# Kernel tuning notes

Hardware: AMD Instinct MI355X
Metric: run time of the kernel (lower is better)

Reference implementation:

```python
import jax, jax.numpy as jnp
import numpy as np

B, S = 4096, 4096
TAU = 0.95
METRIC = 'f1'


def setup_inputs() -> dict:
    key = jax.random.key(0)
    k1, k2 = jax.random.split(key)
    # predicted per-position probabilities, kept strictly positive for log()
    output = jax.random.uniform(k1, (B, S, 1), dtype=jnp.float32, minval=1e-3, maxval=1.0)
    labels = (jax.random.uniform(k2, (B, S)) < 0.2).astype(jnp.float32)
    return {"output": output, "labels": labels}


def _metric_weights(labels):
    # cutoff j keeps documents [0..j] -> prefix statistics via a single cumsum per row
    tp = jnp.cumsum(labels, axis=1)                      # true positives at each cutoff, [B,S]
    if METRIC == 'f1':
        k = jnp.arange(1, labels.shape[1] + 1, dtype=labels.dtype)  # cutoff sizes 1..S
        prec = tp / k                                    # [B,S]
        total = jnp.sum(labels, axis=1, keepdims=True)   # [B,1]
        rec = jnp.where(total > 0, tp / jnp.maximum(total, 1.0), 0.0)
        denom = prec + rec
        r = jnp.where(denom > 0, 2.0 * prec * rec / jnp.maximum(denom, 1e-30), 0.0)
    else:  # dcg
        pos = jnp.arange(labels.shape[1], dtype=labels.dtype)
        gains = labels / jnp.log2(pos + 2.0)             # gain of doc at rank i
        r = jnp.cumsum(gains, axis=1)                    # dcg@(j+1), [B,S]
    return r


def reference(output, labels):
    r = _metric_weights(labels)                          # [B,S]
    q = jnp.exp(r / TAU)                                 # [B,S]
    norm_factor = jnp.sum(q, axis=1, keepdims=True)      # [B,1]
    # NOTE: faithful to original code: q is overwritten with 1/norm_factor
    w = 1.0 / norm_factor                                # [B,1]
    log_out = jnp.log(jnp.squeeze(output, axis=2))       # [B,S]
    loss_matrix = log_out * w                            # broadcast [B,S]*[B,1]
    return -jnp.sum(loss_matrix) / output.shape[0]
```

## Files before the change

### kernel.cpp

```cpp
#include <hip/hip_runtime.h>


#define BDIM 256
#define VPT 16
#define SROW 4096
#define NROWS 4096

__global__ __launch_bounds__(BDIM) void attncut_row_kernel(
    const float* __restrict__ output,
    const float* __restrict__ labels,
    float* __restrict__ row_out)
{
    const int b    = blockIdx.x;
    const int tid  = threadIdx.x;
    const int lane = tid & 63;
    const int wave = tid >> 6;
    const int base = tid * VPT;

    const float* lab = labels + (size_t)b * SROW + base;
    const float* out = output + (size_t)b * SROW + base;

    float4 Lv[4], Ov[4];
    #pragma unroll
    for (int i = 0; i < 4; ++i) Lv[i] = reinterpret_cast<const float4*>(lab)[i];
    #pragma unroll
    for (int i = 0; i < 4; ++i) Ov[i] = reinterpret_cast<const float4*>(out)[i];

    float v[VPT], o[VPT];
    #pragma unroll
    for (int i = 0; i < 4; ++i) {
        v[4*i+0] = Lv[i].x; v[4*i+1] = Lv[i].y; v[4*i+2] = Lv[i].z; v[4*i+3] = Lv[i].w;
        o[4*i+0] = Ov[i].x; o[4*i+1] = Ov[i].y; o[4*i+2] = Ov[i].z; o[4*i+3] = Ov[i].w;
    }

    float pre[VPT];
    float acc = 0.f;
    #pragma unroll
    for (int i = 0; i < VPT; ++i) { acc += v[i]; pre[i] = acc; }
    const float cnt = acc;

    float lsum = 0.f;
    #pragma unroll
    for (int i = 0; i < VPT; ++i) lsum += __logf(o[i]);

    float sc = cnt;
    #pragma unroll
    for (int d = 1; d < 64; d <<= 1) {
        float n = __shfl_up(sc, d, 64);
        if (lane >= d) sc += n;
    }

    __shared__ float wtot[4], wpre[4];
    __shared__ float s_total;
    if (lane == 63) wtot[wave] = sc;
    __syncthreads();
    if (tid == 0) {
        float a = 0.f;
        #pragma unroll
        for (int w = 0; w < 4; ++w) { wpre[w] = a; a += wtot[w]; }
        s_total = a;
    }
    __syncthreads();
    const float total = s_total;
    const float excl  = wpre[wave] + (sc - cnt);

    const float c = 2.0f / 0.95f;
    float qsum = 0.f;
    #pragma unroll
    for (int i = 0; i < VPT; ++i) {
        float tp = excl + pre[i];
        float kf = (float)(base + i + 1) + total;
        qsum += __expf(c * tp * __builtin_amdgcn_rcpf(kf));
    }

    #pragma unroll
    for (int d = 32; d > 0; d >>= 1) {
        qsum += __shfl_down(qsum, d, 64);
        lsum += __shfl_down(lsum, d, 64);
    }
    __shared__ float sq[4], sl[4];
    if (lane == 0) { sq[wave] = qsum; sl[wave] = lsum; }
    __syncthreads();
    if (tid == 0) {
        float Q = 0.f, L = 0.f;
        #pragma unroll
        for (int w = 0; w < 4; ++w) { Q += sq[w]; L += sl[w]; }
        row_out[b] = L / Q;
    }
}

__global__ __launch_bounds__(1024) void attncut_final_kernel(
    const float* __restrict__ row_out, float* __restrict__ d_out)
{
    const int tid = threadIdx.x;
    float s = 0.f;
    for (int i = tid; i < NROWS; i += 1024) s += row_out[i];
    #pragma unroll
    for (int d = 32; d > 0; d >>= 1) s += __shfl_down(s, d, 64);
    __shared__ float sm[16];
    const int lane = tid & 63, wave = tid >> 6;
    if (lane == 0) sm[wave] = s;
    __syncthreads();
    if (tid == 0) {
        float t = 0.f;
        #pragma unroll
        for (int w = 0; w < 16; ++w) t += sm[w];
        d_out[0] = -t / (float)NROWS;
    }
}

extern "C" void kernel_launch(void* const* d_in, const int* in_sizes, int n_in,
                              void* d_out, int out_size, void* d_ws, size_t ws_size,
                              hipStream_t stream) {
    const float* output = (const float*)d_in[0];
    const float* labels = (const float*)d_in[1];
    float* out  = (float*)d_out;
    float* rows = (float*)d_ws;

    attncut_row_kernel<<<NROWS, BDIM, 0, stream>>>(output, labels, rows);
    attncut_final_kernel<<<1, 1024, 0, stream>>>(rows, out);
}
```

Measured before the change: 28.26 us.

## Use one wave per row with ballot/mbcnt prefix counts instead of block scan

Each row is now handled by a single 64-lane wavefront that reads 16 coalesced float4 chunks, strided so the wave covers contiguous 1 KB spans. The labels' prefix sums are computed with ballot and mbcnt bit counts, which removes the shuffle scan, shared memory and both block barriers. The output loads are split into two halves so the second half is fetched while the exp work runs. The trade-off is more registers per thread and fewer threads per row, and the ballot-based count assumes the labels are exactly 0 or 1.

```diff
diff --git a/kernel.cpp b/kernel.cpp
--- a/kernel.cpp
+++ b/kernel.cpp
@@ -1,92 +1,92 @@
 #include <hip/hip_runtime.h>
 
 
-#define BDIM 256
-#define VPT 16
 #define SROW 4096
 #define NROWS 4096
+#define NCHUNK 16
 
-__global__ __launch_bounds__(BDIM) void attncut_row_kernel(
+__global__ __launch_bounds__(64, 4) void attncut_row_kernel(
     const float* __restrict__ output,
     const float* __restrict__ labels,
     float* __restrict__ row_out)
 {
     const int b    = blockIdx.x;
-    const int tid  = threadIdx.x;
-    const int lane = tid & 63;
-    const int wave = tid >> 6;
-    const int base = tid * VPT;
+    const int lane = threadIdx.x;
 
-    const float* lab = labels + (size_t)b * SROW + base;
-    const float* out = output + (size_t)b * SROW + base;
+    const float4* lab4 = reinterpret_cast<const float4*>(labels) + (size_t)b * (SROW / 4) + lane;
+    const float4* out4 = reinterpret_cast<const float4*>(output) + (size_t)b * (SROW / 4) + lane;
 
-    float4 Lv[4], Ov[4];
+    float4 L[NCHUNK];
     #pragma unroll
-    for (int i = 0; i < 4; ++i) Lv[i] = reinterpret_cast<const float4*>(lab)[i];
+    for (int c = 0; c < NCHUNK; ++c) L[c] = lab4[c * 64];
+
+    float4 O0[8];
     #pragma unroll
-    for (int i = 0; i < 4; ++i) Ov[i] = reinterpret_cast<const float4*>(out)[i];
+    for (int c = 0; c < 8; ++c) O0[c] = out4[c * 64];
 
-    float v[VPT], o[VPT];
+    float T[NCHUNK][4];
+    float P[NCHUNK];
+    unsigned int run = 0;
     #pragma unroll
-    for (int i = 0; i < 4; ++i) {
-        v[4*i+0] = Lv[i].x; v[4*i+1] = Lv[i].y; v[4*i+2] = Lv[i].z; v[4*i+3] = Lv[i].w;
-        o[4*i+0] = Ov[i].x; o[4*i+1] = Ov[i].y; o[4*i+2] = Ov[i].z; o[4*i+3] = Ov[i].w;
+    for (int c = 0; c < NCHUNK; ++c) {
+        unsigned long long b0 = __ballot(L[c].x > 0.5f);
+        unsigned long long b1 = __ballot(L[c].y > 0.5f);
+        unsigned long long b2 = __ballot(L[c].z > 0.5f);
+        unsigned long long b3 = __ballot(L[c].w > 0.5f);
+        unsigned int acc = __builtin_amdgcn_mbcnt_lo((unsigned int)b0, 0u);
+        acc = __builtin_amdgcn_mbcnt_hi((unsigned int)(b0 >> 32), acc);
+        acc = __builtin_amdgcn_mbcnt_lo((unsigned int)b1, acc);
+        acc = __builtin_amdgcn_mbcnt_hi((unsigned int)(b1 >> 32), acc);
+        acc = __builtin_amdgcn_mbcnt_lo((unsigned int)b2, acc);
+        acc = __builtin_amdgcn_mbcnt_hi((unsigned int)(b2 >> 32), acc);
+        acc = __builtin_amdgcn_mbcnt_lo((unsigned int)b3, acc);
+        acc = __builtin_amdgcn_mbcnt_hi((unsigned int)(b3 >> 32), acc);
+        float below = (float)acc;
+        float p0 = L[c].x;
+        float p1 = p0 + L[c].y;
+        float p2 = p1 + L[c].z;
+        float p3 = p2 + L[c].w;
+        T[c][0] = below + p0;
+        T[c][1] = below + p1;
+        T[c][2] = below + p2;
+        T[c][3] = below + p3;
+        P[c] = (float)run;
+        run += (unsigned int)(__popcll(b0) + __popcll(b1) + __popcll(b2) + __popcll(b3));
     }
-
-    float pre[VPT];
-    float acc = 0.f;
-    #pragma unroll
-    for (int i = 0; i < VPT; ++i) { acc += v[i]; pre[i] = acc; }
-    const float cnt = acc;
+    const float total = (float)run;
 
     float lsum = 0.f;
     #pragma unroll
-    for (int i = 0; i < VPT; ++i) lsum += __logf(o[i]);
+    for (int c = 0; c < 8; ++c)
+        lsum += __logf(O0[c].x) + __logf(O0[c].y) + __logf(O0[c].z) + __logf(O0[c].w);
 
-    float sc = cnt;
+    float4 O1[8];
     #pragma unroll
-    for (int d = 1; d < 64; d <<= 1) {
-        float n = __shfl_up(sc, d, 64);
-        if (lane >= d) sc += n;
+    for (int c = 0; c < 8; ++c) O1[c] = out4[(c + 8) * 64];
+
+    const float cst   = 2.0f / 0.95f;
+    const float kbase = (float)(lane * 4 + 1) + total;
+    float qsum = 0.f;
+    #pragma unroll
+    for (int c = 0; c < NCHUNK; ++c) {
+        #pragma unroll
+        for (int j = 0; j < 4; ++j) {
+            float tp = P[c] + T[c][j];
+            float kf = kbase + (float)(c * 256 + j);
+            qsum += __expf(cst * tp * __builtin_amdgcn_rcpf(kf));
+        }
     }
 
-    __shared__ float wtot[4], wpre[4];
-    __shared__ float s_total;
-    if (lane == 63) wtot[wave] = sc;
-    __syncthreads();
-    if (tid == 0) {
-        float a = 0.f;
-        #pragma unroll
-        for (int w = 0; w < 4; ++w) { wpre[w] = a; a += wtot[w]; }
-        s_total = a;
-    }
-    __syncthreads();
-    const float total = s_total;
-    const float excl  = wpre[wave] + (sc - cnt);
-
-    const float c = 2.0f / 0.95f;
-    float qsum = 0.f;
     #pragma unroll
-    for (int i = 0; i < VPT; ++i) {
-        float tp = excl + pre[i];
-        float kf = (float)(base + i + 1) + total;
-        qsum += __expf(c * tp * __builtin_amdgcn_rcpf(kf));
-    }
+    for (int c = 0; c < 8; ++c)
+        lsum += __logf(O1[c].x) + __logf(O1[c].y) + __logf(O1[c].z) + __logf(O1[c].w);
 
     #pragma unroll
     for (int d = 32; d > 0; d >>= 1) {
         qsum += __shfl_down(qsum, d, 64);
         lsum += __shfl_down(lsum, d, 64);
     }
-    __shared__ float sq[4], sl[4];
-    if (lane == 0) { sq[wave] = qsum; sl[wave] = lsum; }
-    __syncthreads();
-    if (tid == 0) {
-        float Q = 0.f, L = 0.f;
-        #pragma unroll
-        for (int w = 0; w < 4; ++w) { Q += sq[w]; L += sl[w]; }
-        row_out[b] = L / Q;
-    }
+    if (lane == 0) row_out[b] = lsum / qsum;
 }
 
 __global__ __launch_bounds__(1024) void attncut_final_kernel(
@@ -117,6 +117,6 @@
     float* out  = (float*)d_out;
     float* rows = (float*)d_ws;
 
-    attncut_row_kernel<<<NROWS, BDIM, 0, stream>>>(output, labels, rows);
+    attncut_row_kernel<<<NROWS, 64, 0, stream>>>(output, labels, rows);
     attncut_final_kernel<<<1, 1024, 0, stream>>>(rows, out);
 }
```

Result: slower. 35.73 us (+26.4%).

## Process two rows per block with prefetch of next row's labels

Applied to the files above, without the earlier changes.

Each 256-thread block now handles two consecutive rows instead of one, halving the grid size. While the current row is processed, it loads the next row's labels into registers. The output loads are moved later, after the label prefix sum, so they overlap with the block scan. It also adds a min-blocks-per-CU hint to launch bounds. The aim is to hide memory latency and spread block launch cost in this bandwidth-bound reduction, at the risk of fewer blocks in flight and more register pressure.

```diff
diff --git a/kernel.cpp b/kernel.cpp
--- a/kernel.cpp
+++ b/kernel.cpp
@@ -3,89 +3,108 @@
 
 #define BDIM 256
 #define VPT 16
+#define ROWSPB 2
 #define SROW 4096
 #define NROWS 4096
 
-__global__ __launch_bounds__(BDIM) void attncut_row_kernel(
+__global__ __launch_bounds__(BDIM, 6) void attncut_row_kernel(
     const float* __restrict__ output,
     const float* __restrict__ labels,
     float* __restrict__ row_out)
 {
-    const int b    = blockIdx.x;
     const int tid  = threadIdx.x;
     const int lane = tid & 63;
     const int wave = tid >> 6;
     const int base = tid * VPT;
+    const int r0   = blockIdx.x * ROWSPB;
 
-    const float* lab = labels + (size_t)b * SROW + base;
-    const float* out = output + (size_t)b * SROW + base;
+    const float4* lab4 = reinterpret_cast<const float4*>(labels + (size_t)r0 * SROW + base);
+    const float4* out4 = reinterpret_cast<const float4*>(output + (size_t)r0 * SROW + base);
+    const int ROWSTRIDE = SROW / 4;
 
-    float4 Lv[4], Ov[4];
+    __shared__ float wtot[4], wpre[4], s_total;
+    __shared__ float sq[4], sl[4];
+
+    float4 Lc[4];
     #pragma unroll
-    for (int i = 0; i < 4; ++i) Lv[i] = reinterpret_cast<const float4*>(lab)[i];
-    #pragma unroll
-    for (int i = 0; i < 4; ++i) Ov[i] = reinterpret_cast<const float4*>(out)[i];
-
-    float v[VPT], o[VPT];
-    #pragma unroll
-    for (int i = 0; i < 4; ++i) {
-        v[4*i+0] = Lv[i].x; v[4*i+1] = Lv[i].y; v[4*i+2] = Lv[i].z; v[4*i+3] = Lv[i].w;
-        o[4*i+0] = Ov[i].x; o[4*i+1] = Ov[i].y; o[4*i+2] = Ov[i].z; o[4*i+3] = Ov[i].w;
-    }
-
-    float pre[VPT];
-    float acc = 0.f;
-    #pragma unroll
-    for (int i = 0; i < VPT; ++i) { acc += v[i]; pre[i] = acc; }
-    const float cnt = acc;
-
-    float lsum = 0.f;
-    #pragma unroll
-    for (int i = 0; i < VPT; ++i) lsum += __logf(o[i]);
-
-    float sc = cnt;
-    #pragma unroll
-    for (int d = 1; d < 64; d <<= 1) {
-        float n = __shfl_up(sc, d, 64);
-        if (lane >= d) sc += n;
-    }
-
-    __shared__ float wtot[4], wpre[4];
-    __shared__ float s_total;
-    if (lane == 63) wtot[wave] = sc;
-    __syncthreads();
-    if (tid == 0) {
-        float a = 0.f;
-        #pragma unroll
-        for (int w = 0; w < 4; ++w) { wpre[w] = a; a += wtot[w]; }
-        s_total = a;
-    }
-    __syncthreads();
-    const float total = s_total;
-    const float excl  = wpre[wave] + (sc - cnt);
-
-    const float c = 2.0f / 0.95f;
-    float qsum = 0.f;
-    #pragma unroll
-    for (int i = 0; i < VPT; ++i) {
-        float tp = excl + pre[i];
-        float kf = (float)(base + i + 1) + total;
-        qsum += __expf(c * tp * __builtin_amdgcn_rcpf(kf));
-    }
+    for (int i = 0; i < 4; ++i) Lc[i] = lab4[i];
 
     #pragma unroll
-    for (int d = 32; d > 0; d >>= 1) {
-        qsum += __shfl_down(qsum, d, 64);
-        lsum += __shfl_down(lsum, d, 64);
-    }
-    __shared__ float sq[4], sl[4];
-    if (lane == 0) { sq[wave] = qsum; sl[wave] = lsum; }
-    __syncthreads();
-    if (tid == 0) {
-        float Q = 0.f, L = 0.f;
+    for (int r = 0; r < ROWSPB; ++r) {
+        float4 Ln[4];
+        if (r + 1 < ROWSPB) {
+            #pragma unroll
+            for (int i = 0; i < 4; ++i) Ln[i] = lab4[(r + 1) * ROWSTRIDE + i];
+        }
+
+        float pre[VPT];
+        {
+            float v[VPT];
+            #pragma unroll
+            for (int i = 0; i < 4; ++i) {
+                v[4*i+0] = Lc[i].x; v[4*i+1] = Lc[i].y; v[4*i+2] = Lc[i].z; v[4*i+3] = Lc[i].w;
+            }
+            float acc = 0.f;
+            #pragma unroll
+            for (int i = 0; i < VPT; ++i) { acc += v[i]; pre[i] = acc; }
+        }
+        const float cnt = pre[VPT - 1];
+
+        float4 Ov[4];
         #pragma unroll
-        for (int w = 0; w < 4; ++w) { Q += sq[w]; L += sl[w]; }
-        row_out[b] = L / Q;
+        for (int i = 0; i < 4; ++i) Ov[i] = out4[r * ROWSTRIDE + i];
+
+        float sc = cnt;
+        #pragma unroll
+        for (int d = 1; d < 64; d <<= 1) {
+            float n = __shfl_up(sc, d, 64);
+            if (lane >= d) sc += n;
+        }
+
+        if (lane == 63) wtot[wave] = sc;
+        __syncthreads();
+        if (tid == 0) {
+            float a = 0.f;
+            #pragma unroll
+            for (int w = 0; w < 4; ++w) { wpre[w] = a; a += wtot[w]; }
+            s_total = a;
+        }
+        __syncthreads();
+        const float total = s_total;
+        const float excl  = wpre[wave] + (sc - cnt);
+
+        const float c = 2.0f / 0.95f;
+        float qsum = 0.f;
+        #pragma unroll
+        for (int i = 0; i < VPT; ++i) {
+            float tp = excl + pre[i];
+            float kf = (float)(base + i + 1) + total;
+            qsum += __expf(c * tp * __builtin_amdgcn_rcpf(kf));
+        }
+
+        float lsum = 0.f;
+        #pragma unroll
+        for (int i = 0; i < 4; ++i)
+            lsum += __logf(Ov[i].x) + __logf(Ov[i].y) + __logf(Ov[i].z) + __logf(Ov[i].w);
+
+        #pragma unroll
+        for (int d = 32; d > 0; d >>= 1) {
+            qsum += __shfl_down(qsum, d, 64);
+            lsum += __shfl_down(lsum, d, 64);
+        }
+        if (lane == 0) { sq[wave] = qsum; sl[wave] = lsum; }
+        __syncthreads();
+        if (tid == 0) {
+            float Q = 0.f, L = 0.f;
+            #pragma unroll
+            for (int w = 0; w < 4; ++w) { Q += sq[w]; L += sl[w]; }
+            row_out[r0 + r] = L / Q;
+        }
+
+        if (r + 1 < ROWSPB) {
+            #pragma unroll
+            for (int i = 0; i < 4; ++i) Lc[i] = Ln[i];
+        }
     }
 }
 
@@ -117,6 +136,6 @@
     float* out  = (float*)d_out;
     float* rows = (float*)d_ws;
 
-    attncut_row_kernel<<<NROWS, BDIM, 0, stream>>>(output, labels, rows);
+    attncut_row_kernel<<<NROWS / ROWSPB, BDIM, 0, stream>>>(output, labels, rows);
     attncut_final_kernel<<<1, 1024, 0, stream>>>(rows, out);
 }
```

Measured after the change: 29.16 us. 3.2% more time.
